# Kernel optimization log

Hardware: AMD Instinct MI355X
Metric: run time of the kernel (lower is better)

Reference implementation:

```python
import jax, jax.numpy as jnp
import numpy as np


def setup_inputs() -> dict:
    key = jax.random.key(0)
    k1, k2 = jax.random.split(key)
    data = jax.random.normal(k1, (16, 64, 128, 128), dtype=jnp.float32)
    weights = jax.random.normal(k2, (128, 64, 3, 3), dtype=jnp.float32)
    return {"data": data, "weights": weights}


def reference(data, weights):
    # Original module performs im2col (unfold+reshape) + matmul, which is
    # mathematically a stride-1 VALID cross-correlation in NCHW layout.
    # weights: [C_out, C_in, kH, kW]; output: [B, C_out, H-kH+1, W-kW+1]
    return jax.lax.conv_general_dilated(
        data, weights,
        window_strides=(1, 1),
        padding="VALID",
        dimension_numbers=("NCHW", "OIHW", "NCHW"),
    )
```

## Files before the change

kernel.cpp:

```cpp
#include <hip/hip_runtime.h>


#define BATCH 16
#define CIN   64
#define HIN   128
#define WIN   128
#define COUT  128
#define HO    126
#define WO    126

typedef short bf16x8 __attribute__((ext_vector_type(8)));
typedef float f32x4  __attribute__((ext_vector_type(4)));

__device__ __forceinline__ unsigned short f2bf(float f) {
    union { float f; unsigned int u; } v; v.f = f;
    unsigned int u = v.u;
    unsigned int r = (u + 0x7fffu + ((u >> 16) & 1u)) >> 16;
    return (unsigned short)r;
}

__device__ __forceinline__ void async16(const void* g, void* l) {
    __builtin_amdgcn_global_load_lds(
        (const __attribute__((address_space(1))) unsigned int*)(unsigned long long)g,
        (__attribute__((address_space(3))) unsigned int*)(unsigned long long)l,
        16, 0, 0);
}

__global__ __launch_bounds__(256) void t2_weights(
        const float* __restrict__ w, unsigned short* __restrict__ wt) {
    const int idx = blockIdx.x * 256 + threadIdx.x;
    if (idx < COUT * CIN * 9) {
        const int co = idx / (CIN * 9);
        const int r  = idx % (CIN * 9);
        const int ci = r / 9;
        const int k  = r % 9;
        wt[((size_t)k * COUT + co) * CIN + ci] = f2bf(w[idx]);
    }
}

__global__ __launch_bounds__(512, 4) void conv_fused(
        const float* __restrict__ x,
        const unsigned short* __restrict__ wt,
        float* __restrict__ out) {
    __shared__ __align__(16) char smem[26112 + 32768];
    short* halo = (short*)smem;
    short* As   = (short*)(smem + 26112);

    const int raw = (blockIdx.z * 126 + blockIdx.y) * 2 + blockIdx.x;
    const int s = (raw & 7) * 504 + (raw >> 3);
    const int b  = s / 252;
    const int r2 = s - b * 252;
    const int oh = r2 >> 1;
    const int W0 = (r2 & 1) * 64;

    const int tid  = threadIdx.x;
    const int lane = tid & 63, wid = tid >> 6;
    const int co0  = (wid & 3) * 32;
    const int n0   = (wid >> 2) * 32;
    const int col  = lane & 15, quad = lane >> 4;
    const int swl = (lane * 16) ^ ((lane >> 3) << 4);

    const int tw = tid & 63, oct = tid >> 6;
    float v[3][8];
    {
        const float* xb = x + ((size_t)b * CIN + oct * 8) * (HIN * WIN)
                            + (size_t)oh * WIN + W0 + tw;
#pragma unroll
        for (int kh = 0; kh < 3; kh++)
#pragma unroll
            for (int j = 0; j < 8; j++)
                v[kh][j] = xb[(size_t)j * (HIN * WIN) + kh * WIN];
    }
    float tv[8];
    const int oct2 = tid & 7, tw2 = 64 + ((tid >> 3) & 3), tkh = tid >> 5;
    if (tid < 96) {
        int wi = W0 + tw2; if (wi > WIN - 1) wi = WIN - 1;
        const float* xb2 = x + ((size_t)b * CIN + oct2 * 8) * (HIN * WIN)
                             + (size_t)(oh + tkh) * WIN + wi;
#pragma unroll
        for (int j = 0; j < 8; j++)
            tv[j] = xb2[(size_t)j * (HIN * WIN)];
    }

    {
        const char* srcA = (const char*)wt;
        char* dstA = (char*)As;
#pragma unroll
        for (int i = 0; i < 2; i++) {
            const int c = wid * 2 + i;
            async16(srcA + c * 1024 + swl, dstA + c * 1024 + lane * 16);
        }
    }

#pragma unroll
    for (int kh = 0; kh < 3; kh++) {
        bf16x8 p;
#pragma unroll
        for (int j = 0; j < 8; j++) p[j] = (short)f2bf(v[kh][j]);
        const int r = kh * 68 + tw;
        *(bf16x8*)((char*)halo + ((r * 128 + oct * 16) ^ ((r & 7) << 4))) = p;
    }
    if (tid < 96) {
        bf16x8 p;
#pragma unroll
        for (int j = 0; j < 8; j++) p[j] = (short)f2bf(tv[j]);
        const int r = tkh * 68 + tw2;
        *(bf16x8*)((char*)halo + ((r * 128 + oct2 * 16) ^ ((r & 7) << 4))) = p;
    }

    __syncthreads();

    f32x4 acc[2][2] = {};

#pragma unroll
    for (int t = 0; t < 9; t++) {
        const int kh = t / 3, kw = t - kh * 3;
        if (t + 1 < 9) {
            const char* srcA = (const char*)wt + (size_t)(t + 1) * 16384;
            char* dstA = (char*)As + ((t + 1) & 1) * 16384;
#pragma unroll
            for (int i = 0; i < 2; i++) {
                const int c = wid * 2 + i;
                async16(srcA + c * 1024 + swl, dstA + c * 1024 + lane * 16);
            }
        }
        const short* At = As + (t & 1) * 8192;
#pragma unroll
        for (int kk = 0; kk < 2; kk++) {
            bf16x8 aa[2], bb[2];
#pragma unroll
            for (int mi = 0; mi < 2; mi++) {
                const int r = co0 + mi * 16 + col;
                aa[mi] = *(const bf16x8*)&At[(r * 64 + kk * 32 + quad * 8) ^ ((r & 7) << 3)];
            }
#pragma unroll
            for (int ni = 0; ni < 2; ni++) {
                const int r = kh * 68 + n0 + ni * 16 + col + kw;
                bb[ni] = *(const bf16x8*)&halo[(r * 64 + kk * 32 + quad * 8) ^ ((r & 7) << 3)];
            }
#pragma unroll
            for (int mi = 0; mi < 2; mi++)
#pragma unroll
                for (int ni = 0; ni < 2; ni++)
                    acc[mi][ni] = __builtin_amdgcn_mfma_f32_16x16x32_bf16(
                        aa[mi], bb[ni], acc[mi][ni], 0, 0, 0);
        }
        if (t + 1 < 9) __syncthreads();
    }

#pragma unroll
    for (int ni = 0; ni < 2; ni++) {
        const int ow = W0 + n0 + ni * 16 + col;
        if (ow < WO) {
#pragma unroll
            for (int mi = 0; mi < 2; mi++) {
                const int co = co0 + mi * 16 + quad * 4;
                float* o = out + (((size_t)b * COUT + co) * HO + oh) * WO + ow;
#pragma unroll
                for (int r = 0; r < 4; r++)
                    o[(size_t)r * HO * WO] = acc[mi][ni][r];
            }
        }
    }
}

__global__ __launch_bounds__(256) void conv_direct(
        const float* __restrict__ x, const float* __restrict__ w,
        float* __restrict__ y) {
    const int idx = blockIdx.x * 256 + threadIdx.x;
    if (idx >= BATCH * COUT * HO * WO) return;
    const int ow = idx % WO;
    int t = idx / WO;
    const int oh = t % HO; t /= HO;
    const int co = t % COUT;
    const int b  = t / COUT;
    float acc = 0.f;
    const float* xb = x + (((size_t)b * CIN) * HIN + oh) * WIN + ow;
    const float* wc = w + (size_t)co * (CIN * 9);
    for (int ci = 0; ci < CIN; ci++) {
#pragma unroll
        for (int kh = 0; kh < 3; kh++)
#pragma unroll
            for (int kw = 0; kw < 3; kw++)
                acc += xb[(size_t)ci * (HIN * WIN) + kh * WIN + kw] * wc[ci * 9 + kh * 3 + kw];
    }
    y[idx] = acc;
}

extern "C" void kernel_launch(void* const* d_in, const int* in_sizes, int n_in,
                              void* d_out, int out_size, void* d_ws, size_t ws_size,
                              hipStream_t stream) {
    const float* data    = (const float*)d_in[0];
    const float* weights = (const float*)d_in[1];
    float* out = (float*)d_out;

    const size_t wt_bytes = (size_t)9 * COUT * CIN * 2;

    if (ws_size >= wt_bytes) {
        unsigned short* wt = (unsigned short*)d_ws;
        t2_weights<<<(COUT * CIN * 9 + 255) / 256, 256, 0, stream>>>(weights, wt);
        conv_fused<<<dim3(2, 126, BATCH), 512, 0, stream>>>(data, wt, out);
    } else {
        const int n = BATCH * COUT * HO * WO;
        conv_direct<<<(n + 255) / 256, 256, 0, stream>>>(data, weights, out);
    }
}
```

Measured before the change: 232.1 us.

## Compute two output rows per block to reuse halo and weight tiles

Each block now produces two output rows instead of one. It loads a 4-row input halo in place of 3, and each wave covers 64 output channels by 32 output columns with a larger accumulator array. The grid is halved, so every weight tile staged through LDS serves twice as many outputs and the shared halo rows are loaded once rather than twice. The cost is more LDS and more accumulator registers per thread, which may lower occupancy, and fewer blocks in the grid.

```diff
diff --git a/kernel.cpp b/kernel.cpp
--- a/kernel.cpp
+++ b/kernel.cpp
@@ -42,41 +42,44 @@
         const float* __restrict__ x,
         const unsigned short* __restrict__ wt,
         float* __restrict__ out) {
-    __shared__ __align__(16) char smem[26112 + 32768];
+    __shared__ __align__(16) char smem[34816 + 32768];
     short* halo = (short*)smem;
-    short* As   = (short*)(smem + 26112);
-
-    const int raw = (blockIdx.z * 126 + blockIdx.y) * 2 + blockIdx.x;
-    const int s = (raw & 7) * 504 + (raw >> 3);
-    const int b  = s / 252;
-    const int r2 = s - b * 252;
-    const int oh = r2 >> 1;
-    const int W0 = (r2 & 1) * 64;
+    short* As   = (short*)(smem + 34816);
+
+    const int raw = (blockIdx.z * 63 + blockIdx.y) * 2 + blockIdx.x;
+    const int s = (raw & 7) * 252 + (raw >> 3);
+    const int b   = s / 126;
+    const int r2  = s - b * 126;
+    const int ohp = r2 >> 1;
+    const int oh0 = ohp * 2;
+    const int W0  = (r2 & 1) * 64;
 
     const int tid  = threadIdx.x;
     const int lane = tid & 63, wid = tid >> 6;
-    const int co0  = (wid & 3) * 32;
-    const int n0   = (wid >> 2) * 32;
+    const int co0  = (wid & 1) * 64;
+    const int sg   = (wid >> 1) & 3;
+    const int ohq  = sg >> 1;
+    const int ow0  = (sg & 1) * 32;
     const int col  = lane & 15, quad = lane >> 4;
     const int swl = (lane * 16) ^ ((lane >> 3) << 4);
 
     const int tw = tid & 63, oct = tid >> 6;
-    float v[3][8];
+    float v[4][8];
     {
         const float* xb = x + ((size_t)b * CIN + oct * 8) * (HIN * WIN)
-                            + (size_t)oh * WIN + W0 + tw;
-#pragma unroll
-        for (int kh = 0; kh < 3; kh++)
+                            + (size_t)oh0 * WIN + W0 + tw;
+#pragma unroll
+        for (int hr = 0; hr < 4; hr++)
 #pragma unroll
             for (int j = 0; j < 8; j++)
-                v[kh][j] = xb[(size_t)j * (HIN * WIN) + kh * WIN];
+                v[hr][j] = xb[(size_t)j * (HIN * WIN) + hr * WIN];
     }
     float tv[8];
-    const int oct2 = tid & 7, tw2 = 64 + ((tid >> 3) & 3), tkh = tid >> 5;
-    if (tid < 96) {
+    const int tw2 = 64 + (tid & 3), oct2 = (tid >> 2) & 7, hr2 = tid >> 5;
+    if (tid < 128) {
         int wi = W0 + tw2; if (wi > WIN - 1) wi = WIN - 1;
         const float* xb2 = x + ((size_t)b * CIN + oct2 * 8) * (HIN * WIN)
-                             + (size_t)(oh + tkh) * WIN + wi;
+                             + (size_t)(oh0 + hr2) * WIN + wi;
 #pragma unroll
         for (int j = 0; j < 8; j++)
             tv[j] = xb2[(size_t)j * (HIN * WIN)];
@@ -93,24 +96,24 @@
     }
 
 #pragma unroll
-    for (int kh = 0; kh < 3; kh++) {
+    for (int hr = 0; hr < 4; hr++) {
         bf16x8 p;
 #pragma unroll
-        for (int j = 0; j < 8; j++) p[j] = (short)f2bf(v[kh][j]);
-        const int r = kh * 68 + tw;
+        for (int j = 0; j < 8; j++) p[j] = (short)f2bf(v[hr][j]);
+        const int r = hr * 68 + tw;
         *(bf16x8*)((char*)halo + ((r * 128 + oct * 16) ^ ((r & 7) << 4))) = p;
     }
-    if (tid < 96) {
+    if (tid < 128) {
         bf16x8 p;
 #pragma unroll
         for (int j = 0; j < 8; j++) p[j] = (short)f2bf(tv[j]);
-        const int r = tkh * 68 + tw2;
+        const int r = hr2 * 68 + tw2;
         *(bf16x8*)((char*)halo + ((r * 128 + oct2 * 16) ^ ((r & 7) << 4))) = p;
     }
 
     __syncthreads();
 
-    f32x4 acc[2][2] = {};
+    f32x4 acc[4][2] = {};
 
 #pragma unroll
     for (int t = 0; t < 9; t++) {
@@ -127,19 +130,19 @@
         const short* At = As + (t & 1) * 8192;
 #pragma unroll
         for (int kk = 0; kk < 2; kk++) {
-            bf16x8 aa[2], bb[2];
-#pragma unroll
-            for (int mi = 0; mi < 2; mi++) {
+            bf16x8 aa[4], bb[2];
+#pragma unroll
+            for (int mi = 0; mi < 4; mi++) {
                 const int r = co0 + mi * 16 + col;
                 aa[mi] = *(const bf16x8*)&At[(r * 64 + kk * 32 + quad * 8) ^ ((r & 7) << 3)];
             }
 #pragma unroll
             for (int ni = 0; ni < 2; ni++) {
-                const int r = kh * 68 + n0 + ni * 16 + col + kw;
+                const int r = (ohq + kh) * 68 + ow0 + ni * 16 + col + kw;
                 bb[ni] = *(const bf16x8*)&halo[(r * 64 + kk * 32 + quad * 8) ^ ((r & 7) << 3)];
             }
 #pragma unroll
-            for (int mi = 0; mi < 2; mi++)
+            for (int mi = 0; mi < 4; mi++)
 #pragma unroll
                 for (int ni = 0; ni < 2; ni++)
                     acc[mi][ni] = __builtin_amdgcn_mfma_f32_16x16x32_bf16(
@@ -148,12 +151,13 @@
         if (t + 1 < 9) __syncthreads();
     }
 
+    const int oh = oh0 + ohq;
 #pragma unroll
     for (int ni = 0; ni < 2; ni++) {
-        const int ow = W0 + n0 + ni * 16 + col;
+        const int ow = W0 + ow0 + ni * 16 + col;
         if (ow < WO) {
 #pragma unroll
-            for (int mi = 0; mi < 2; mi++) {
+            for (int mi = 0; mi < 4; mi++) {
                 const int co = co0 + mi * 16 + quad * 4;
                 float* o = out + (((size_t)b * COUT + co) * HO + oh) * WO + ow;
 #pragma unroll
@@ -199,7 +203,7 @@
     if (ws_size >= wt_bytes) {
         unsigned short* wt = (unsigned short*)d_ws;
         t2_weights<<<(COUT * CIN * 9 + 255) / 256, 256, 0, stream>>>(weights, wt);
-        conv_fused<<<dim3(2, 126, BATCH), 512, 0, stream>>>(data, wt, out);
+        conv_fused<<<dim3(2, 63, BATCH), 512, 0, stream>>>(data, wt, out);
     } else {
         const int n = BATCH * COUT * HO * WO;
         conv_direct<<<(n + 255) / 256, 256, 0, stream>>>(data, weights, out);
```

New measurement: 212.1 us. 8.6% less time.
